# Kernel tuning notes

Hardware: AMD Instinct MI355X
Metric: run time of the kernel (lower is better)

The kernel has to match this reference:

```python
import jax, jax.numpy as jnp
import numpy as np

N = 50000
E = 1600000
F_IN = 256
HEADS = 4
HID = 32
C = 16
NEG_SLOPE = 0.2


def _add_self_loops(edge_index, n):
    loop = jnp.arange(n, dtype=edge_index.dtype)
    return jnp.concatenate([edge_index, jnp.stack([loop, loop])], axis=1)


def gat_conv(x, edge_index, W, att_src, att_dst, bias, heads, n):
    # PyG GATConv (concat=True, add_self_loops=True, inference: no dropout)
    ei = _add_self_loops(edge_index, n)
    src, dst = ei[0], ei[1]
    d = W.shape[1] // heads
    xw = (x @ W).reshape(n, heads, d)                      # [N,H,D]
    a_src = jnp.sum(xw * att_src, axis=-1)                 # [N,H]
    a_dst = jnp.sum(xw * att_dst, axis=-1)                 # [N,H]
    e = jax.nn.leaky_relu(a_src[src] + a_dst[dst], NEG_SLOPE)  # [E',H]
    # segment softmax over destination neighborhoods
    m = jax.ops.segment_max(e, dst, num_segments=n)        # [N,H]
    ex = jnp.exp(e - m[dst])
    denom = jax.ops.segment_sum(ex, dst, num_segments=n)   # [N,H]
    alpha = ex / denom[dst]                                # [E',H]
    msg = xw[src] * alpha[:, :, None]                      # [E',H,D]
    out = jax.ops.segment_sum(msg, dst, num_segments=n)    # [N,H,D]
    return out.reshape(n, heads * d) + bias


def setup_inputs() -> dict:
    key = jax.random.key(0)
    ks = jax.random.split(key, 10)
    g = lambda k, shape, fan: jax.random.normal(k, shape, jnp.float32) * (1.0 / np.sqrt(fan))
    x = jax.random.normal(ks[0], (N, F_IN), jnp.float32)
    edge_index = jax.random.randint(ks[1], (2, E), 0, N, dtype=jnp.int64)
    return {
        "x": x,
        "edge_index": edge_index,
        "W1": g(ks[2], (F_IN, HEADS * HID), F_IN),
        "att_src1": g(ks[3], (HEADS, HID), HID),
        "att_dst1": g(ks[4], (HEADS, HID), HID),
        "b1": jnp.zeros((HEADS * HID,), jnp.float32),
        "W2": g(ks[5], (HEADS * HID, C), HEADS * HID),
        "att_src2": g(ks[6], (1, C), C),
        "att_dst2": g(ks[7], (1, C), C),
        "b2": jnp.zeros((C,), jnp.float32),
    }


def reference(x, edge_index, W1, att_src1, att_dst1, b1, W2, att_src2, att_dst2, b2):
    h = gat_conv(x, edge_index, W1, att_src1, att_dst1, b1, HEADS, N)
    h = jax.nn.relu(h)
    # dropout: identity at inference (training=False)
    out = gat_conv(h, edge_index, W2, att_src2, att_dst2, b2, 1, N)
    return jax.nn.log_softmax(out, axis=1)
```

## Files before the change

kernel.cpp:

```cpp
#include <hip/hip_runtime.h>
#include <hip/hip_bf16.h>

typedef __hip_bfloat16 bf16;
typedef long long i64;
typedef unsigned long long u64;
typedef __attribute__((ext_vector_type(8))) short short8;
typedef __attribute__((ext_vector_type(4))) float floatx4;

#define NN    50000
#define EE    1600000
#define E2    1650000
#define FIN   256
#define HD    128
#define NH    4
#define NC    16
#define SLOPE 0.2f
#define K     128
#define DPB   391
#define CAPB  16384
#define CAP   15360
#define CH2   2048

#define FR_W  36
#define FW_W  68

#define OF_FLAGS 0
#define OF_BCUR  16
#define OF_BBASE 144
#define OF_RP    280
#define OF_BIN   50282
#define OF_CSR   4244586
#define OF_XQ    5894588
#define OF_SC    7494588
#define OF_AS1   9094588
#define OF_AD1   9294588
#define OF_HW2   9494588
#define OF_AS2   10294588
#define OF_AD2   10344588

__device__ __forceinline__ float b2f(bf16 v) { return __bfloat162float(v); }
__device__ __forceinline__ float us2f(unsigned short u) {
    return __uint_as_float(((unsigned)u) << 16);
}
__device__ __forceinline__ unsigned short f2us(float f) {
    unsigned u = __float_as_uint(f);
    return (unsigned short)((u + 0x7fffu + ((u >> 16) & 1u)) >> 16);
}
__device__ __forceinline__ float lrelu(float v) { return v > 0.f ? v : SLOPE * v; }
__device__ __forceinline__ float sb2f(unsigned u, int sh) {
    return (float)((int)(u << (24 - sh)) >> 24);
}

template <bool F32>
__device__ __forceinline__ float ldin(const void* p, int i) {
    if (F32) return ((const float*)p)[i];
    return b2f(((const bf16*)p)[i]);
}
template <bool F32>
__device__ __forceinline__ float4 ldin4(const void* p, int i) {
    if (F32) return *(const float4*)((const float*)p + i);
    ushort4 u = *(const ushort4*)((const unsigned short*)p + i);
    float4 r;
    r.x = us2f(u.x); r.y = us2f(u.y); r.z = us2f(u.z); r.w = us2f(u.w);
    return r;
}

__device__ __forceinline__ void edge_sd(const void* ei, int f64, int e, int& s, int& d) {
    if (e >= EE) { s = e - EE; d = s; return; }
    if (f64) {
        s = (int)((const i64*)ei)[e];
        d = (int)((const i64*)ei)[EE + e];
    } else {
        s = ((const int*)ei)[e];
        d = ((const int*)ei)[EE + e];
    }
    s = min(max(s, 0), NN - 1);
    d = min(max(d, 0), NN - 1);
}

__global__ void detect(const void* x, const void* ei, int* flags, int* bcur) {
    __shared__ int cnt[2];
    int t = threadIdx.x;
    if (t < K) bcur[t] = t * CAPB;
    if (t == 0) { cnt[0] = 0; cnt[1] = 0; }
    __syncthreads();
    const unsigned short* xb = (const unsigned short*)x;
    int c0 = 0;
    for (int i = t; i < 4096; i += 256) {
        float v = __uint_as_float(((unsigned)xb[2 * i]) << 16);
        if (!(fabsf(v) < 1e6f)) c0++;
    }
    const i64* e64 = (const i64*)ei;
    int c1 = 0;
    for (int i = t; i < 1024; i += 256) {
        i64 v = e64[i];
        if (v >= 0 && v < NN) c1++;
    }
    atomicAdd(&cnt[0], c0);
    atomicAdd(&cnt[1], c1);
    __syncthreads();
    if (t == 0) {
        flags[0] = (cnt[0] > 400) ? 1 : 0;
        flags[1] = (cnt[1] >= 1000) ? 1 : 0;
    }
}

__global__ __launch_bounds__(256) void binScatter(const void* __restrict__ ei,
                                                  const int* __restrict__ flags,
                                                  int* __restrict__ bcur,
                                                  u64* __restrict__ bin) {
    __shared__ int h[K], res[K];
    int t = threadIdx.x;
    int base = blockIdx.x * CH2 + t * 8;
    if (t < K) h[t] = 0;
    __syncthreads();
    int f64 = flags[1];
    int sv[8], dv[8], rk[8];
    int n_ = 0;
    if (!f64 && base + 8 <= EE) {
        const int* es = (const int*)ei;
        int4 a = *(const int4*)&es[base];
        int4 b = *(const int4*)&es[base + 4];
        int4 c = *(const int4*)&es[EE + base];
        int4 g = *(const int4*)&es[EE + base + 4];
        sv[0] = a.x; sv[1] = a.y; sv[2] = a.z; sv[3] = a.w;
        sv[4] = b.x; sv[5] = b.y; sv[6] = b.z; sv[7] = b.w;
        dv[0] = c.x; dv[1] = c.y; dv[2] = c.z; dv[3] = c.w;
        dv[4] = g.x; dv[5] = g.y; dv[6] = g.z; dv[7] = g.w;
#pragma unroll
        for (int i = 0; i < 8; i++) {
            sv[i] = min(max(sv[i], 0), NN - 1);
            dv[i] = min(max(dv[i], 0), NN - 1);
        }
        n_ = 8;
    } else {
        for (int i = 0; i < 8; i++) {
            int e = base + i;
            if (e < E2) {
                int s, d; edge_sd(ei, f64, e, s, d);
                sv[n_] = s; dv[n_] = d; n_++;
            }
        }
    }
#pragma unroll 8
    for (int i = 0; i < n_; i++) rk[i] = atomicAdd(&h[dv[i] / DPB], 1);
    __syncthreads();
    if (t < K) res[t] = h[t] ? atomicAdd(&bcur[t], h[t]) : 0;
    __syncthreads();
#pragma unroll 8
    for (int i = 0; i < n_; i++) {
        int b = dv[i] / DPB;
        int pos = res[b] + rk[i];
        pos = min(pos, (b + 1) * CAPB - 1);
        bin[pos] = (((u64)(unsigned)dv[i]) << 32) | (unsigned)sv[i];
    }
}

__global__ void bucketScan(const int* __restrict__ bcur, int* __restrict__ bbase) {
    __shared__ int sh[K];
    int t = threadIdx.x;
    int v = min(bcur[t] - t * CAPB, CAPB);
    sh[t] = v;
    __syncthreads();
    for (int off = 1; off < K; off <<= 1) {
        int u = (t >= off) ? sh[t - off] : 0;
        __syncthreads();
        sh[t] += u;
        __syncthreads();
    }
    bbase[t] = sh[t] - v;
    if (t == K - 1) bbase[K] = sh[K - 1];
}

__global__ __launch_bounds__(256) void csrB(const u64* __restrict__ bin,
                                            const int* __restrict__ bbase,
                                            int* __restrict__ rp, int* __restrict__ csr) {
    __shared__ int cnt[512];
    __shared__ int cur[DPB];
    __shared__ int buf[CAP];
    int b = blockIdx.x, t = threadIdx.x;
    int d0 = b * DPB;
    int nd = min(DPB, NN - d0);
    int src0 = b * CAPB;
    int base = bbase[b], size = bbase[b + 1] - base;
    cnt[t] = 0; cnt[t + 256] = 0;
    __syncthreads();
    for (int i = t; i < size; i += 256) {
        int d = (int)(bin[src0 + i] >> 32);
        atomicAdd(&cnt[d - d0], 1);
    }
    __syncthreads();
    int a0 = cnt[2 * t], a1 = cnt[2 * t + 1];
    int ps = a0 + a1;
    buf[t] = ps;
    __syncthreads();
    for (int off = 1; off < 256; off <<= 1) {
        int u = (t >= off) ? buf[t - off] : 0;
        __syncthreads();
        buf[t] += u;
        __syncthreads();
    }
    int ex = buf[t] - ps;
    __syncthreads();
    cnt[2 * t] = ex;
    cnt[2 * t + 1] = ex + a0;
    __syncthreads();
    for (int i = t; i < nd; i += 256) {
        rp[d0 + i] = base + cnt[i];
        cur[i] = cnt[i];
    }
    if (b == K - 1 && t == 0) rp[NN] = bbase[K];
    __syncthreads();
    if (size <= CAP) {
        for (int i = t; i < size; i += 256) {
            u64 p = bin[src0 + i];
            int pos = atomicAdd(&cur[(int)(p >> 32) - d0], 1);
            buf[pos] = (int)(unsigned)p;
        }
        __syncthreads();
        for (int i = t; i < size; i += 256) csr[base + i] = buf[i];
    } else {
        for (int i = t; i < size; i += 256) {
            u64 p = bin[src0 + i];
            int pos = base + atomicAdd(&cur[(int)(p >> 32) - d0], 1);
            csr[pos] = (int)(unsigned)p;
        }
    }
}

template <bool F32>
__global__ __launch_bounds__(256) void gemm1(
    const void* __restrict__ x, const void* __restrict__ W1,
    const void* __restrict__ as1, const void* __restrict__ ad1,
    const int* __restrict__ flags, signed char* __restrict__ xq, float* __restrict__ sc2,
    float* __restrict__ asrc, float* __restrict__ adst) {
    if ((flags[0] != 0) != F32) return;
    __shared__ unsigned short af[8 * 64 * FR_W];
    __shared__ unsigned short wb[8 * 64 * FR_W];
    __shared__ float scl[64];
    int t = threadIdx.x;
    int mb = blockIdx.x >> 1, nb = blockIdx.x & 1;
    int m0 = mb * 64, n0 = nb * 64;
#pragma unroll
    for (int i = 0; i < 16; i++) {
        int slot = i * 256 + t;
        int mi = slot >> 6, k4 = (slot & 63) * 4;
        float4 v = make_float4(0.f, 0.f, 0.f, 0.f);
        if (m0 + mi < NN) v = ldin4<F32>(x, (m0 + mi) * FIN + k4);
        ushort4 o;
        o.x = f2us(v.x); o.y = f2us(v.y); o.z = f2us(v.z); o.w = f2us(v.w);
        *(ushort4*)&af[((k4 >> 5) * 64 + mi) * FR_W + (k4 & 31)] = o;
    }
#pragma unroll
    for (int i = 0; i < 16; i++) {
        int k = i * 16 + (t >> 4);
        int ni = (t & 15) * 4;
        float4 v = ldin4<F32>(W1, k * HD + n0 + ni);
        int ks = k >> 5, kk = k & 31;
        wb[(ks * 64 + ni + 0) * FR_W + kk] = f2us(v.x);
        wb[(ks * 64 + ni + 1) * FR_W + kk] = f2us(v.y);
        wb[(ks * 64 + ni + 2) * FR_W + kk] = f2us(v.z);
        wb[(ks * 64 + ni + 3) * FR_W + kk] = f2us(v.w);
    }
    __syncthreads();
    int w = t >> 6, lane = t & 63;
    int col = lane & 15, q = lane >> 4;
    floatx4 dacc[4];
#pragma unroll
    for (int mt = 0; mt < 4; mt++) { dacc[mt].x = 0.f; dacc[mt].y = 0.f; dacc[mt].z = 0.f; dacc[mt].w = 0.f; }
#pragma unroll
    for (int ks = 0; ks < 8; ks++) {
        short8 bf = *(const short8*)&wb[(ks * 64 + w * 16 + col) * FR_W + q * 8];
#pragma unroll
        for (int mt = 0; mt < 4; mt++) {
            short8 afr = *(const short8*)&af[(ks * 64 + mt * 16 + col) * FR_W + q * 8];
            dacc[mt] = __builtin_amdgcn_mfma_f32_16x16x32_bf16(afr, bf, dacc[mt], 0, 0, 0);
        }
    }
    __syncthreads();
    float* fw = (float*)af;
#pragma unroll
    for (int mt = 0; mt < 4; mt++) {
#pragma unroll
        for (int r = 0; r < 4; r++) {
            int nloc = mt * 16 + q * 4 + r;
            fw[nloc * FW_W + w * 16 + col] = dacc[mt][r];
        }
    }
    __syncthreads();
    {
        int node = t >> 2, part = t & 3;
        float amax = 0.f;
#pragma unroll
        for (int c = 0; c < 16; c++) amax = fmaxf(amax, fabsf(fw[node * FW_W + part * 16 + c]));
        amax = fmaxf(amax, __shfl_xor(amax, 1));
        amax = fmaxf(amax, __shfl_xor(amax, 2));
        if (part == 0) {
            scl[node] = (amax > 0.f) ? 127.f / amax : 0.f;
            if (m0 + node < NN) sc2[(m0 + node) * 2 + nb] = amax * (1.f / 127.f);
        }
    }
    __syncthreads();
    {
        int node = t >> 2, part = t & 3;
        if (m0 + node < NN) {
            float inv = scl[node];
            unsigned dw[4];
#pragma unroll
            for (int g = 0; g < 4; g++) {
                unsigned pk = 0;
#pragma unroll
                for (int j = 0; j < 4; j++) {
                    float v = fw[node * FW_W + part * 16 + g * 4 + j];
                    int qi = (int)rintf(v * inv);
                    qi = min(127, max(-127, qi));
                    pk |= ((unsigned)(qi & 255)) << (8 * j);
                }
                dw[g] = pk;
            }
            *(uint4*)&xq[(m0 + node) * HD + n0 + part * 16] = make_uint4(dw[0], dw[1], dw[2], dw[3]);
        }
    }
    {
        int node = t >> 2, hh = (t >> 1) & 1, half = t & 1;
        if (m0 + node < NN) {
            float s = 0.f, dd = 0.f;
            int cb = hh * 32 + half * 16;
#pragma unroll
            for (int c = 0; c < 16; c++) {
                float xv = fw[node * FW_W + cb + c];
                s  += xv * ldin<F32>(as1, n0 + cb + c);
                dd += xv * ldin<F32>(ad1, n0 + cb + c);
            }
            s  += __shfl_xor(s, 1);
            dd += __shfl_xor(dd, 1);
            if (half == 0) {
                int head = nb * 2 + hh;
                asrc[(m0 + node) * NH + head] = s;
                adst[(m0 + node) * NH + head] = dd;
            }
        }
    }
}

template <bool F32>
__global__ __launch_bounds__(128) void node1(
    const int* __restrict__ rp, const int* __restrict__ cs,
    const float* __restrict__ asrc, const float* __restrict__ adst,
    const signed char* __restrict__ xq, const float* __restrict__ sc2,
    const void* __restrict__ b1, const void* __restrict__ W2,
    const void* __restrict__ as2, const void* __restrict__ ad2,
    const int* __restrict__ flags, float* __restrict__ hw2,
    float* __restrict__ asrc2, float* __restrict__ adst2) {
    if ((flags[0] != 0) != F32) return;
    int d = blockIdx.x, t = threadIdx.x;
    int beg = rp[d], end = rp[d + 1];
    __shared__ float sw[32][4];
    __shared__ int   ss[32];
    __shared__ float red[2][HD];
    __shared__ float wv[2][4];
    __shared__ float hs[HD];
    __shared__ float l2[32];
    int hw_ = t & 3;
    float adw = adst[d * NH + hw_];
    int cg = t & 15, eo = t >> 4, head = cg >> 2;
    float acc[8];
#pragma unroll
    for (int j = 0; j < 8; j++) acc[j] = 0.f;
    float wacc = 0.f;
    const unsigned* xqu = (const unsigned*)xq;
    for (int chb = beg; chb < end; chb += 32) {
        __syncthreads();
        int ec = chb + (t >> 2);
        float w = 0.f, wsc = 0.f;
        int s = 0;
        if (ec < end) {
            s = cs[ec];
            w = __expf(fminf(lrelu(asrc[s * NH + hw_] + adw), 80.f));
            wsc = w * sc2[s * 2 + (hw_ >> 1)];
        }
        sw[t >> 2][hw_] = wsc;
        if (hw_ == 0) ss[t >> 2] = s;
        wacc += w;
        __syncthreads();
        int m = min(32, end - chb);
        for (int e = eo; e < m; e += 8) {
            float we = sw[e][head];
            int s2 = ss[e];
            uint2 u = *(const uint2*)&xqu[s2 * 32 + cg * 2];
            acc[0] += we * sb2f(u.x, 0);
            acc[1] += we * sb2f(u.x, 8);
            acc[2] += we * sb2f(u.x, 16);
            acc[3] += we * sb2f(u.x, 24);
            acc[4] += we * sb2f(u.y, 0);
            acc[5] += we * sb2f(u.y, 8);
            acc[6] += we * sb2f(u.y, 16);
            acc[7] += we * sb2f(u.y, 24);
        }
    }
    wacc += __shfl_xor(wacc, 4);
    wacc += __shfl_xor(wacc, 8);
    wacc += __shfl_xor(wacc, 16);
    wacc += __shfl_xor(wacc, 32);
    int wid = t >> 6, lane = t & 63;
    if (lane < 4) wv[wid][lane] = wacc;
#pragma unroll
    for (int j = 0; j < 8; j++) {
        acc[j] += __shfl_xor(acc[j], 16);
        acc[j] += __shfl_xor(acc[j], 32);
    }
    if (lane < 16) {
#pragma unroll
        for (int j = 0; j < 8; j++) red[wid][lane * 8 + j] = acc[j];
    }
    __syncthreads();
    float tot = red[0][t] + red[1][t];
    float wt  = wv[0][t >> 5] + wv[1][t >> 5];
    hs[t] = fmaxf(tot / wt + ldin<F32>(b1, t), 0.f);
    __syncthreads();
    int j = t & 15, g = t >> 4;
    float p = 0.f;
#pragma unroll
    for (int k = 0; k < 16; k++) p += hs[g * 16 + k] * ldin<F32>(W2, (g * 16 + k) * NC + j);
    p += __shfl_xor(p, 16, 64);
    p += __shfl_xor(p, 32, 64);
    if ((t & 63) < 16) l2[(t >> 6) * 16 + j] = p;
    __syncthreads();
    if (t < 16) {
        float hw = l2[t] + l2[16 + t];
        hw2[d * NC + t] = hw;
        float a2s = hw * ldin<F32>(as2, t);
        float a2d = hw * ldin<F32>(ad2, t);
#pragma unroll
        for (int off = 8; off; off >>= 1) {
            a2s += __shfl_xor(a2s, off, 16);
            a2d += __shfl_xor(a2d, off, 16);
        }
        if (t == 0) { asrc2[d] = a2s; adst2[d] = a2d; }
    }
}

template <bool F32>
__global__ __launch_bounds__(64) void node2(
    const int* __restrict__ rp, const int* __restrict__ cs,
    const float* __restrict__ asrc2, const float* __restrict__ adst2,
    const float* __restrict__ hw2, const void* __restrict__ b2,
    const int* __restrict__ flags, void* __restrict__ out) {
    if ((flags[0] != 0) != F32) return;
    int d = blockIdx.x, t = threadIdx.x;
    int beg = rp[d], end = rp[d + 1];
    float ad = adst2[d];
    __shared__ float sw2[64];
    __shared__ int   ss2[64];
    int q = t & 3, eo = t >> 2;
    float4 acc = make_float4(0.f, 0.f, 0.f, 0.f);
    float wsum = 0.f;
    for (int chb = beg; chb < end; chb += 64) {
        __syncthreads();
        int ec = chb + t;
        float w = 0.f;
        int s = 0;
        if (ec < end) {
            s = cs[ec];
            w = __expf(fminf(lrelu(asrc2[s] + ad), 80.f));
        }
        sw2[t] = w;
        ss2[t] = s;
        __syncthreads();
        int m = min(64, end - chb);
        for (int e = eo; e < m; e += 16) {
            float we = sw2[e];
            float4 v = *(const float4*)&hw2[ss2[e] * NC + q * 4];
            acc.x += we * v.x; acc.y += we * v.y;
            acc.z += we * v.z; acc.w += we * v.w;
            wsum += we;
        }
    }
#pragma unroll
    for (int off = 4; off < 64; off <<= 1) {
        acc.x += __shfl_xor(acc.x, off);
        acc.y += __shfl_xor(acc.y, off);
        acc.z += __shfl_xor(acc.z, off);
        acc.w += __shfl_xor(acc.w, off);
        wsum  += __shfl_xor(wsum, off);
    }
    float rw = 1.f / wsum;
    float v0 = acc.x * rw + ldin<F32>(b2, q * 4 + 0);
    float v1 = acc.y * rw + ldin<F32>(b2, q * 4 + 1);
    float v2 = acc.z * rw + ldin<F32>(b2, q * 4 + 2);
    float v3 = acc.w * rw + ldin<F32>(b2, q * 4 + 3);
    float mx = fmaxf(fmaxf(v0, v1), fmaxf(v2, v3));
    mx = fmaxf(mx, __shfl_xor(mx, 1));
    mx = fmaxf(mx, __shfl_xor(mx, 2));
    float es = __expf(v0 - mx) + __expf(v1 - mx) + __expf(v2 - mx) + __expf(v3 - mx);
    es += __shfl_xor(es, 1);
    es += __shfl_xor(es, 2);
    float lse = mx + __logf(es);
    if (t < 4) {
        if (F32) {
            *(float4*)&((float*)out)[d * NC + q * 4] =
                make_float4(v0 - lse, v1 - lse, v2 - lse, v3 - lse);
        } else {
            bf16* o = (bf16*)out + d * NC + q * 4;
            o[0] = __float2bfloat16(v0 - lse); o[1] = __float2bfloat16(v1 - lse);
            o[2] = __float2bfloat16(v2 - lse); o[3] = __float2bfloat16(v3 - lse);
        }
    }
}

extern "C" void kernel_launch(void* const* d_in, const int* in_sizes, int n_in,
                              void* d_out, int out_size, void* d_ws, size_t ws_size,
                              hipStream_t stream) {
    const void* x   = d_in[0];
    const void* ei  = d_in[1];
    const void* W1  = d_in[2];
    const void* as1 = d_in[3];
    const void* ad1 = d_in[4];
    const void* b1  = d_in[5];
    const void* W2  = d_in[6];
    const void* as2 = d_in[7];
    const void* ad2 = d_in[8];
    const void* b2v = d_in[9];

    float* ws = (float*)d_ws;
    int* flags = (int*)(ws + OF_FLAGS);
    int* bcur  = (int*)(ws + OF_BCUR);
    int* bbase = (int*)(ws + OF_BBASE);
    int* rp    = (int*)(ws + OF_RP);
    u64* bin   = (u64*)(ws + OF_BIN);
    int* csr   = (int*)(ws + OF_CSR);
    signed char* xq = (signed char*)(ws + OF_XQ);
    float* sc2   = ws + OF_SC;
    float* asrc1 = ws + OF_AS1;
    float* adst1 = ws + OF_AD1;
    float* hw2   = ws + OF_HW2;
    float* asrc2 = ws + OF_AS2;
    float* adst2 = ws + OF_AD2;

    detect<<<1, 256, 0, stream>>>(x, ei, flags, bcur);
    binScatter<<<(E2 + CH2 - 1) / CH2, 256, 0, stream>>>(ei, flags, bcur, bin);
    bucketScan<<<1, K, 0, stream>>>(bcur, bbase);
    csrB<<<K, 256, 0, stream>>>(bin, bbase, rp, csr);

    const int GB = ((NN + 63) / 64) * 2;
    gemm1<true><<<GB, 256, 0, stream>>>(x, W1, as1, ad1, flags, xq, sc2, asrc1, adst1);
    node1<true><<<NN, 128, 0, stream>>>(rp, csr, asrc1, adst1, xq, sc2, b1, W2, as2, ad2,
                                        flags, hw2, asrc2, adst2);
    node2<true><<<NN, 64, 0, stream>>>(rp, csr, asrc2, adst2, hw2, b2v, flags, d_out);
}
```

Measured before the change: 306.2 us.

## Split layer-1 aggregation into per-half-head passes with wave-per-node and separate W2 kernel

Splits the int8 projected features into two 64-column halves so each of two aggregation passes gathers a smaller per-node working set that better fits in cache. Each wavefront handles one destination node, using ds_bpermute for broadcast instead of shared memory and block barriers. The W2 projection and layer-2 attention scores move into a separate kernel that handles 16 nodes per block with W2 cached in LDS. This costs an extra bf16 round trip for the hidden activations, reads the CSR twice, and adds kernel launches.

```diff
diff --git a/kernel.cpp b/kernel.cpp
--- a/kernel.cpp
+++ b/kernel.cpp
@@ -27,16 +27,19 @@
 #define OF_FLAGS 0
 #define OF_BCUR  16
 #define OF_BBASE 144
-#define OF_RP    280
-#define OF_BIN   50282
-#define OF_CSR   4244586
-#define OF_XQ    5894588
-#define OF_SC    7494588
-#define OF_AS1   9094588
-#define OF_AD1   9294588
-#define OF_HW2   9494588
-#define OF_AS2   10294588
-#define OF_AD2   10344588
+#define OF_RP    304
+#define OF_BIN   50308
+#define OF_HA    50308
+#define OF_HB    1650308
+#define OF_CSR   4244612
+#define OF_XQA   5894612
+#define OF_XQB   6694612
+#define OF_SC    7494612
+#define OF_AS1   7594612
+#define OF_AD1   7794612
+#define OF_HW2   7994612
+#define OF_AS2   8794612
+#define OF_AD2   8844612
 
 __device__ __forceinline__ float b2f(bf16 v) { return __bfloat162float(v); }
 __device__ __forceinline__ float us2f(unsigned short u) {
@@ -49,6 +52,12 @@
 __device__ __forceinline__ float lrelu(float v) { return v > 0.f ? v : SLOPE * v; }
 __device__ __forceinline__ float sb2f(unsigned u, int sh) {
     return (float)((int)(u << (24 - sh)) >> 24);
+}
+__device__ __forceinline__ float bpermf(int srcLane, float v) {
+    return __int_as_float(__builtin_amdgcn_ds_bpermute(srcLane * 4, __float_as_int(v)));
+}
+__device__ __forceinline__ int bpermi(int srcLane, int v) {
+    return __builtin_amdgcn_ds_bpermute(srcLane * 4, v);
 }
 
 template <bool F32>
@@ -232,9 +241,10 @@
 __global__ __launch_bounds__(256) void gemm1(
     const void* __restrict__ x, const void* __restrict__ W1,
     const void* __restrict__ as1, const void* __restrict__ ad1,
-    const int* __restrict__ flags, signed char* __restrict__ xq, float* __restrict__ sc2,
+    const int* __restrict__ flags, signed char* __restrict__ xqA,
+    signed char* __restrict__ xqB, float* __restrict__ sc2,
     float* __restrict__ asrc, float* __restrict__ adst) {
-    if ((flags[0] != 0) != F32) return;
+    if (flags[0] != (F32 ? 1 : 0)) return;
     __shared__ unsigned short af[8 * 64 * FR_W];
     __shared__ unsigned short wb[8 * 64 * FR_W];
     __shared__ float scl[64];
@@ -318,7 +328,8 @@
                 }
                 dw[g] = pk;
             }
-            *(uint4*)&xq[(m0 + node) * HD + n0 + part * 16] = make_uint4(dw[0], dw[1], dw[2], dw[3]);
+            signed char* xqH = nb ? xqB : xqA;
+            *(uint4*)&xqH[(m0 + node) * 64 + part * 16] = make_uint4(dw[0], dw[1], dw[2], dw[3]);
         }
     }
     {
@@ -343,101 +354,116 @@
     }
 }
 
-template <bool F32>
-__global__ __launch_bounds__(128) void node1(
+template <bool F32, int HALF>
+__global__ __launch_bounds__(256) void nodeAgg(
     const int* __restrict__ rp, const int* __restrict__ cs,
     const float* __restrict__ asrc, const float* __restrict__ adst,
-    const signed char* __restrict__ xq, const float* __restrict__ sc2,
-    const void* __restrict__ b1, const void* __restrict__ W2,
-    const void* __restrict__ as2, const void* __restrict__ ad2,
-    const int* __restrict__ flags, float* __restrict__ hw2,
-    float* __restrict__ asrc2, float* __restrict__ adst2) {
-    if ((flags[0] != 0) != F32) return;
-    int d = blockIdx.x, t = threadIdx.x;
+    const signed char* __restrict__ xqH, const float* __restrict__ sc2,
+    const void* __restrict__ b1, const int* __restrict__ flags,
+    unsigned short* __restrict__ hH) {
+    if (flags[0] != (F32 ? 1 : 0)) return;
+    int t = threadIdx.x, wv = t >> 6, lane = t & 63;
+    int d = blockIdx.x * 4 + wv;
     int beg = rp[d], end = rp[d + 1];
-    __shared__ float sw[32][4];
-    __shared__ int   ss[32];
-    __shared__ float red[2][HD];
-    __shared__ float wv[2][4];
-    __shared__ float hs[HD];
-    __shared__ float l2[32];
-    int hw_ = t & 3;
-    float adw = adst[d * NH + hw_];
-    int cg = t & 15, eo = t >> 4, head = cg >> 2;
+    int eloc = lane >> 1, h = lane & 1;
+    int cg = lane & 7, eo = lane >> 3, hl = cg >> 2;
+    float adw = adst[d * NH + HALF * 2 + h];
+    const unsigned* xqu = (const unsigned*)xqH;
     float acc[8];
 #pragma unroll
     for (int j = 0; j < 8; j++) acc[j] = 0.f;
     float wacc = 0.f;
-    const unsigned* xqu = (const unsigned*)xq;
-    for (int chb = beg; chb < end; chb += 32) {
-        __syncthreads();
-        int ec = chb + (t >> 2);
-        float w = 0.f, wsc = 0.f;
+    for (int ch = beg; ch < end; ch += 32) {
+        int idx = ch + eloc;
+        float wsc = 0.f;
         int s = 0;
-        if (ec < end) {
-            s = cs[ec];
-            w = __expf(fminf(lrelu(asrc[s * NH + hw_] + adw), 80.f));
-            wsc = w * sc2[s * 2 + (hw_ >> 1)];
-        }
-        sw[t >> 2][hw_] = wsc;
-        if (hw_ == 0) ss[t >> 2] = s;
-        wacc += w;
-        __syncthreads();
-        int m = min(32, end - chb);
-        for (int e = eo; e < m; e += 8) {
-            float we = sw[e][head];
-            int s2 = ss[e];
-            uint2 u = *(const uint2*)&xqu[s2 * 32 + cg * 2];
-            acc[0] += we * sb2f(u.x, 0);
-            acc[1] += we * sb2f(u.x, 8);
-            acc[2] += we * sb2f(u.x, 16);
-            acc[3] += we * sb2f(u.x, 24);
-            acc[4] += we * sb2f(u.y, 0);
-            acc[5] += we * sb2f(u.y, 8);
-            acc[6] += we * sb2f(u.y, 16);
-            acc[7] += we * sb2f(u.y, 24);
-        }
-    }
+        if (idx < end) {
+            s = cs[idx];
+            float wval = __expf(fminf(lrelu(asrc[s * NH + HALF * 2 + h] + adw), 80.f));
+            wacc += wval;
+            wsc = wval * sc2[s * 2 + HALF];
+        }
+        int m = min(32, end - ch);
+        int rounds = (m + 7) >> 3;
+        for (int r = 0; r < rounds; r++) {
+            int e = eo + r * 8;
+            float we = bpermf(e * 2 + hl, wsc);
+            int s2 = bpermi(e * 2, s);
+            if (e < m) {
+                uint2 u = *(const uint2*)&xqu[s2 * 16 + cg * 2];
+                acc[0] += we * sb2f(u.x, 0);
+                acc[1] += we * sb2f(u.x, 8);
+                acc[2] += we * sb2f(u.x, 16);
+                acc[3] += we * sb2f(u.x, 24);
+                acc[4] += we * sb2f(u.y, 0);
+                acc[5] += we * sb2f(u.y, 8);
+                acc[6] += we * sb2f(u.y, 16);
+                acc[7] += we * sb2f(u.y, 24);
+            }
+        }
+    }
+#pragma unroll
+    for (int j = 0; j < 8; j++) {
+        acc[j] += __shfl_xor(acc[j], 8);
+        acc[j] += __shfl_xor(acc[j], 16);
+        acc[j] += __shfl_xor(acc[j], 32);
+    }
+    wacc += __shfl_xor(wacc, 2);
     wacc += __shfl_xor(wacc, 4);
     wacc += __shfl_xor(wacc, 8);
     wacc += __shfl_xor(wacc, 16);
     wacc += __shfl_xor(wacc, 32);
-    int wid = t >> 6, lane = t & 63;
-    if (lane < 4) wv[wid][lane] = wacc;
-#pragma unroll
-    for (int j = 0; j < 8; j++) {
-        acc[j] += __shfl_xor(acc[j], 16);
-        acc[j] += __shfl_xor(acc[j], 32);
-    }
-    if (lane < 16) {
-#pragma unroll
-        for (int j = 0; j < 8; j++) red[wid][lane * 8 + j] = acc[j];
-    }
-    __syncthreads();
-    float tot = red[0][t] + red[1][t];
-    float wt  = wv[0][t >> 5] + wv[1][t >> 5];
-    hs[t] = fmaxf(tot / wt + ldin<F32>(b1, t), 0.f);
-    __syncthreads();
-    int j = t & 15, g = t >> 4;
-    float p = 0.f;
-#pragma unroll
-    for (int k = 0; k < 16; k++) p += hs[g * 16 + k] * ldin<F32>(W2, (g * 16 + k) * NC + j);
-    p += __shfl_xor(p, 16, 64);
-    p += __shfl_xor(p, 32, 64);
-    if ((t & 63) < 16) l2[(t >> 6) * 16 + j] = p;
-    __syncthreads();
-    if (t < 16) {
-        float hw = l2[t] + l2[16 + t];
-        hw2[d * NC + t] = hw;
-        float a2s = hw * ldin<F32>(as2, t);
-        float a2d = hw * ldin<F32>(ad2, t);
-#pragma unroll
-        for (int off = 8; off; off >>= 1) {
-            a2s += __shfl_xor(a2s, off, 16);
-            a2d += __shfl_xor(a2d, off, 16);
-        }
-        if (t == 0) { asrc2[d] = a2s; adst2[d] = a2d; }
-    }
+    float ws0 = __shfl(wacc, 0), ws1 = __shfl(wacc, 1);
+    if (eo == 0) {
+        float rw = 1.f / (hl ? ws1 : ws0);
+        unsigned pk[4];
+#pragma unroll
+        for (int g = 0; g < 4; g++) {
+            float v0 = fmaxf(acc[2 * g]     * rw + ldin<F32>(b1, HALF * 64 + cg * 8 + 2 * g), 0.f);
+            float v1 = fmaxf(acc[2 * g + 1] * rw + ldin<F32>(b1, HALF * 64 + cg * 8 + 2 * g + 1), 0.f);
+            pk[g] = ((unsigned)f2us(v1) << 16) | f2us(v0);
+        }
+        *(uint4*)&hH[(size_t)d * 64 + cg * 8] = make_uint4(pk[0], pk[1], pk[2], pk[3]);
+    }
+}
+
+template <bool F32>
+__global__ __launch_bounds__(256) void nodeW(
+    const unsigned short* __restrict__ hA, const unsigned short* __restrict__ hB,
+    const void* __restrict__ W2, const void* __restrict__ as2, const void* __restrict__ ad2,
+    const int* __restrict__ flags, float* __restrict__ hw2,
+    float* __restrict__ asrc2, float* __restrict__ adst2) {
+    if (flags[0] != (F32 ? 1 : 0)) return;
+    __shared__ float hs[16][132];
+    __shared__ float w2s[HD * NC];
+    int t = threadIdx.x;
+    int dst0 = blockIdx.x * 16;
+    for (int i = t; i < HD * NC / 4; i += 256)
+        *(float4*)&w2s[i * 4] = ldin4<F32>(W2, i * 4);
+    {
+        int dn = t >> 4, oct = t & 15;
+        uint4 u = (oct < 8) ? ((const uint4*)hA)[(size_t)(dst0 + dn) * 8 + oct]
+                            : ((const uint4*)hB)[(size_t)(dst0 + dn) * 8 + (oct - 8)];
+        float* hp = &hs[dn][oct * 8];
+        hp[0] = us2f((unsigned short)(u.x & 0xffff)); hp[1] = us2f((unsigned short)(u.x >> 16));
+        hp[2] = us2f((unsigned short)(u.y & 0xffff)); hp[3] = us2f((unsigned short)(u.y >> 16));
+        hp[4] = us2f((unsigned short)(u.z & 0xffff)); hp[5] = us2f((unsigned short)(u.z >> 16));
+        hp[6] = us2f((unsigned short)(u.w & 0xffff)); hp[7] = us2f((unsigned short)(u.w >> 16));
+    }
+    __syncthreads();
+    int ln = t >> 4, j = t & 15;
+    float acc = 0.f;
+#pragma unroll 8
+    for (int k = 0; k < HD; k++) acc += hs[ln][k] * w2s[k * NC + j];
+    hw2[(dst0 + ln) * NC + j] = acc;
+    float a2s = acc * ldin<F32>(as2, j);
+    float a2d = acc * ldin<F32>(ad2, j);
+#pragma unroll
+    for (int off = 8; off; off >>= 1) {
+        a2s += __shfl_xor(a2s, off, 16);
+        a2d += __shfl_xor(a2d, off, 16);
+    }
+    if (j == 0) { asrc2[dst0 + ln] = a2s; adst2[dst0 + ln] = a2d; }
 }
 
 template <bool F32>
@@ -446,7 +472,7 @@
     const float* __restrict__ asrc2, const float* __restrict__ adst2,
     const float* __restrict__ hw2, const void* __restrict__ b2,
     const int* __restrict__ flags, void* __restrict__ out) {
-    if ((flags[0] != 0) != F32) return;
+    if (flags[0] != (F32 ? 1 : 0)) return;
     int d = blockIdx.x, t = threadIdx.x;
     int beg = rp[d], end = rp[d + 1];
     float ad = adst2[d];
@@ -529,7 +555,10 @@
     int* rp    = (int*)(ws + OF_RP);
     u64* bin   = (u64*)(ws + OF_BIN);
     int* csr   = (int*)(ws + OF_CSR);
-    signed char* xq = (signed char*)(ws + OF_XQ);
+    signed char* xqA = (signed char*)(ws + OF_XQA);
+    signed char* xqB = (signed char*)(ws + OF_XQB);
+    unsigned short* hA = (unsigned short*)(ws + OF_HA);
+    unsigned short* hB = (unsigned short*)(ws + OF_HB);
     float* sc2   = ws + OF_SC;
     float* asrc1 = ws + OF_AS1;
     float* adst1 = ws + OF_AD1;
@@ -543,8 +572,9 @@
     csrB<<<K, 256, 0, stream>>>(bin, bbase, rp, csr);
 
     const int GB = ((NN + 63) / 64) * 2;
-    gemm1<true><<<GB, 256, 0, stream>>>(x, W1, as1, ad1, flags, xq, sc2, asrc1, adst1);
-    node1<true><<<NN, 128, 0, stream>>>(rp, csr, asrc1, adst1, xq, sc2, b1, W2, as2, ad2,
-                                        flags, hw2, asrc2, adst2);
+    gemm1<true><<<GB, 256, 0, stream>>>(x, W1, as1, ad1, flags, xqA, xqB, sc2, asrc1, adst1);
+    nodeAgg<true, 0><<<NN / 4, 256, 0, stream>>>(rp, csr, asrc1, adst1, xqA, sc2, b1, flags, hA);
+    nodeAgg<true, 1><<<NN / 4, 256, 0, stream>>>(rp, csr, asrc1, adst1, xqB, sc2, b1, flags, hB);
+    nodeW<true><<<NN / 16, 256, 0, stream>>>(hA, hB, W2, as2, ad2, flags, hw2, asrc2, adst2);
     node2<true><<<NN, 64, 0, stream>>>(rp, csr, asrc2, adst2, hw2, b2v, flags, d_out);
 }
```

Result: slower. 324.8 us (+6.1%).

## Pretranspose W1 once and compute full 128-column tile per gemm1 block

Applied to the files above, without the earlier changes.

Adds a small kernel that converts W1 to bf16 in an MFMA-friendly transposed layout in workspace. gemm1 then reads B fragments straight from global memory instead of staging W1 in shared memory. Each block now covers all 128 output columns for its 64 rows, so the x tile is loaded and converted once per row instead of twice. The epilogue, quantization and attention dot products are reworked to match. In exchange, each wave holds more accumulator registers and does more global B-fragment reads.

```diff
diff --git a/kernel.cpp b/kernel.cpp
--- a/kernel.cpp
+++ b/kernel.cpp
@@ -21,22 +21,22 @@
 #define CAP   15360
 #define CH2   2048
 
-#define FR_W  36
-#define FW_W  68
+#define KS_S  2312
 
 #define OF_FLAGS 0
 #define OF_BCUR  16
 #define OF_BBASE 144
 #define OF_RP    280
-#define OF_BIN   50282
-#define OF_CSR   4244586
-#define OF_XQ    5894588
-#define OF_SC    7494588
-#define OF_AS1   9094588
-#define OF_AD1   9294588
-#define OF_HW2   9494588
-#define OF_AS2   10294588
-#define OF_AD2   10344588
+#define OF_W1T   50284
+#define OF_BIN   66668
+#define OF_CSR   4260972
+#define OF_XQ    5910972
+#define OF_SC    7510972
+#define OF_AS1   7610972
+#define OF_AD1   7810972
+#define OF_HW2   8010972
+#define OF_AS2   8810972
+#define OF_AD2   8860972
 
 __device__ __forceinline__ float b2f(bf16 v) { return __bfloat162float(v); }
 __device__ __forceinline__ float us2f(unsigned short u) {
@@ -49,6 +49,9 @@
 __device__ __forceinline__ float lrelu(float v) { return v > 0.f ? v : SLOPE * v; }
 __device__ __forceinline__ float sb2f(unsigned u, int sh) {
     return (float)((int)(u << (24 - sh)) >> 24);
+}
+__device__ __forceinline__ int fwi(int node, int ch) {
+    return node * 132 + (ch >> 5) * 33 + (ch & 31);
 }
 
 template <bool F32>
@@ -103,6 +106,20 @@
         flags[0] = (cnt[0] > 400) ? 1 : 0;
         flags[1] = (cnt[1] >= 1000) ? 1 : 0;
     }
+}
+
+template <bool F32>
+__global__ void trW(const void* __restrict__ W1, const int* __restrict__ flags,
+                    unsigned short* __restrict__ w1t) {
+    if (flags[0] != (F32 ? 1 : 0)) return;
+    int t = blockIdx.x * 256 + threadIdx.x;
+    int k = t >> 5, n4 = (t & 31) * 4;
+    float4 v = ldin4<F32>(W1, k * HD + n4);
+    int ks = k >> 5, kk = k & 31;
+    w1t[((ks * HD + n4 + 0) * 32) + kk] = f2us(v.x);
+    w1t[((ks * HD + n4 + 1) * 32) + kk] = f2us(v.y);
+    w1t[((ks * HD + n4 + 2) * 32) + kk] = f2us(v.z);
+    w1t[((ks * HD + n4 + 3) * 32) + kk] = f2us(v.w);
 }
 
 __global__ __launch_bounds__(256) void binScatter(const void* __restrict__ ei,
@@ -230,17 +247,15 @@
 
 template <bool F32>
 __global__ __launch_bounds__(256) void gemm1(
-    const void* __restrict__ x, const void* __restrict__ W1,
+    const void* __restrict__ x, const unsigned short* __restrict__ w1t,
     const void* __restrict__ as1, const void* __restrict__ ad1,
     const int* __restrict__ flags, signed char* __restrict__ xq, float* __restrict__ sc2,
     float* __restrict__ asrc, float* __restrict__ adst) {
-    if ((flags[0] != 0) != F32) return;
-    __shared__ unsigned short af[8 * 64 * FR_W];
-    __shared__ unsigned short wb[8 * 64 * FR_W];
-    __shared__ float scl[64];
+    if (flags[0] != (F32 ? 1 : 0)) return;
+    __shared__ unsigned short af[8 * KS_S];
+    __shared__ float scl[128];
     int t = threadIdx.x;
-    int mb = blockIdx.x >> 1, nb = blockIdx.x & 1;
-    int m0 = mb * 64, n0 = nb * 64;
+    int m0 = blockIdx.x * 64;
 #pragma unroll
     for (int i = 0; i < 16; i++) {
         int slot = i * 256 + t;
@@ -249,97 +264,77 @@
         if (m0 + mi < NN) v = ldin4<F32>(x, (m0 + mi) * FIN + k4);
         ushort4 o;
         o.x = f2us(v.x); o.y = f2us(v.y); o.z = f2us(v.z); o.w = f2us(v.w);
-        *(ushort4*)&af[((k4 >> 5) * 64 + mi) * FR_W + (k4 & 31)] = o;
-    }
-#pragma unroll
-    for (int i = 0; i < 16; i++) {
-        int k = i * 16 + (t >> 4);
-        int ni = (t & 15) * 4;
-        float4 v = ldin4<F32>(W1, k * HD + n0 + ni);
-        int ks = k >> 5, kk = k & 31;
-        wb[(ks * 64 + ni + 0) * FR_W + kk] = f2us(v.x);
-        wb[(ks * 64 + ni + 1) * FR_W + kk] = f2us(v.y);
-        wb[(ks * 64 + ni + 2) * FR_W + kk] = f2us(v.z);
-        wb[(ks * 64 + ni + 3) * FR_W + kk] = f2us(v.w);
+        *(ushort4*)&af[(k4 >> 5) * KS_S + mi * 36 + (k4 & 31)] = o;
     }
     __syncthreads();
     int w = t >> 6, lane = t & 63;
     int col = lane & 15, q = lane >> 4;
-    floatx4 dacc[4];
-#pragma unroll
-    for (int mt = 0; mt < 4; mt++) { dacc[mt].x = 0.f; dacc[mt].y = 0.f; dacc[mt].z = 0.f; dacc[mt].w = 0.f; }
+    floatx4 acc[4][2];
+#pragma unroll
+    for (int mt = 0; mt < 4; mt++)
+#pragma unroll
+        for (int u = 0; u < 2; u++) { acc[mt][u].x = 0.f; acc[mt][u].y = 0.f; acc[mt][u].z = 0.f; acc[mt][u].w = 0.f; }
 #pragma unroll
     for (int ks = 0; ks < 8; ks++) {
-        short8 bf = *(const short8*)&wb[(ks * 64 + w * 16 + col) * FR_W + q * 8];
+        short8 bf0 = *(const short8*)&w1t[(ks * HD + w * 32 + col) * 32 + q * 8];
+        short8 bf1 = *(const short8*)&w1t[(ks * HD + w * 32 + 16 + col) * 32 + q * 8];
 #pragma unroll
         for (int mt = 0; mt < 4; mt++) {
-            short8 afr = *(const short8*)&af[(ks * 64 + mt * 16 + col) * FR_W + q * 8];
-            dacc[mt] = __builtin_amdgcn_mfma_f32_16x16x32_bf16(afr, bf, dacc[mt], 0, 0, 0);
+            short8 afr = *(const short8*)&af[ks * KS_S + (mt * 16 + col) * 36 + q * 8];
+            acc[mt][0] = __builtin_amdgcn_mfma_f32_16x16x32_bf16(afr, bf0, acc[mt][0], 0, 0, 0);
+            acc[mt][1] = __builtin_amdgcn_mfma_f32_16x16x32_bf16(afr, bf1, acc[mt][1], 0, 0, 0);
         }
     }
     __syncthreads();
     float* fw = (float*)af;
 #pragma unroll
-    for (int mt = 0; mt < 4; mt++) {
-#pragma unroll
-        for (int r = 0; r < 4; r++) {
-            int nloc = mt * 16 + q * 4 + r;
-            fw[nloc * FW_W + w * 16 + col] = dacc[mt][r];
-        }
-    }
-    __syncthreads();
+    for (int mt = 0; mt < 4; mt++)
+#pragma unroll
+        for (int u = 0; u < 2; u++)
+#pragma unroll
+            for (int r = 0; r < 4; r++) {
+                int node = mt * 16 + q * 4 + r;
+                fw[fwi(node, w * 32 + u * 16 + col)] = acc[mt][u][r];
+            }
+    __syncthreads();
+    int node = t >> 2, part = t & 3;
     {
-        int node = t >> 2, part = t & 3;
         float amax = 0.f;
 #pragma unroll
-        for (int c = 0; c < 16; c++) amax = fmaxf(amax, fabsf(fw[node * FW_W + part * 16 + c]));
+        for (int c = 0; c < 32; c++) amax = fmaxf(amax, fabsf(fw[fwi(node, part * 32 + c)]));
         amax = fmaxf(amax, __shfl_xor(amax, 1));
-        amax = fmaxf(amax, __shfl_xor(amax, 2));
-        if (part == 0) {
-            scl[node] = (amax > 0.f) ? 127.f / amax : 0.f;
-            if (m0 + node < NN) sc2[(m0 + node) * 2 + nb] = amax * (1.f / 127.f);
-        }
-    }
-    __syncthreads();
-    {
-        int node = t >> 2, part = t & 3;
-        if (m0 + node < NN) {
-            float inv = scl[node];
-            unsigned dw[4];
-#pragma unroll
-            for (int g = 0; g < 4; g++) {
-                unsigned pk = 0;
-#pragma unroll
-                for (int j = 0; j < 4; j++) {
-                    float v = fw[node * FW_W + part * 16 + g * 4 + j];
-                    int qi = (int)rintf(v * inv);
-                    qi = min(127, max(-127, qi));
-                    pk |= ((unsigned)(qi & 255)) << (8 * j);
-                }
-                dw[g] = pk;
+        if ((part & 1) == 0) {
+            scl[node * 2 + (part >> 1)] = (amax > 0.f) ? 127.f / amax : 0.f;
+            if (m0 + node < NN) sc2[(m0 + node) * 2 + (part >> 1)] = amax * (1.f / 127.f);
+        }
+    }
+    __syncthreads();
+    if (m0 + node < NN) {
+        float inv = scl[node * 2 + (part >> 1)];
+        unsigned dw[8];
+#pragma unroll
+        for (int g = 0; g < 8; g++) {
+            unsigned pk = 0;
+#pragma unroll
+            for (int j = 0; j < 4; j++) {
+                float v = fw[fwi(node, part * 32 + g * 4 + j)];
+                int qi = (int)rintf(v * inv);
+                qi = min(127, max(-127, qi));
+                pk |= ((unsigned)(qi & 255)) << (8 * j);
             }
-            *(uint4*)&xq[(m0 + node) * HD + n0 + part * 16] = make_uint4(dw[0], dw[1], dw[2], dw[3]);
-        }
-    }
-    {
-        int node = t >> 2, hh = (t >> 1) & 1, half = t & 1;
-        if (m0 + node < NN) {
-            float s = 0.f, dd = 0.f;
-            int cb = hh * 32 + half * 16;
-#pragma unroll
-            for (int c = 0; c < 16; c++) {
-                float xv = fw[node * FW_W + cb + c];
-                s  += xv * ldin<F32>(as1, n0 + cb + c);
-                dd += xv * ldin<F32>(ad1, n0 + cb + c);
-            }
-            s  += __shfl_xor(s, 1);
-            dd += __shfl_xor(dd, 1);
-            if (half == 0) {
-                int head = nb * 2 + hh;
-                asrc[(m0 + node) * NH + head] = s;
-                adst[(m0 + node) * NH + head] = dd;
-            }
-        }
+            dw[g] = pk;
+        }
+        *(uint4*)&xq[(m0 + node) * HD + part * 32]      = make_uint4(dw[0], dw[1], dw[2], dw[3]);
+        *(uint4*)&xq[(m0 + node) * HD + part * 32 + 16] = make_uint4(dw[4], dw[5], dw[6], dw[7]);
+        float s = 0.f, dd = 0.f;
+#pragma unroll
+        for (int c = 0; c < 32; c++) {
+            float xv = fw[fwi(node, part * 32 + c)];
+            s  += xv * ldin<F32>(as1, part * 32 + c);
+            dd += xv * ldin<F32>(ad1, part * 32 + c);
+        }
+        asrc[(m0 + node) * NH + part] = s;
+        adst[(m0 + node) * NH + part] = dd;
     }
 }
 
@@ -352,7 +347,7 @@
     const void* __restrict__ as2, const void* __restrict__ ad2,
     const int* __restrict__ flags, float* __restrict__ hw2,
     float* __restrict__ asrc2, float* __restrict__ adst2) {
-    if ((flags[0] != 0) != F32) return;
+    if (flags[0] != (F32 ? 1 : 0)) return;
     int d = blockIdx.x, t = threadIdx.x;
     int beg = rp[d], end = rp[d + 1];
     __shared__ float sw[32][4];
@@ -446,7 +441,7 @@
     const float* __restrict__ asrc2, const float* __restrict__ adst2,
     const float* __restrict__ hw2, const void* __restrict__ b2,
     const int* __restrict__ flags, void* __restrict__ out) {
-    if ((flags[0] != 0) != F32) return;
+    if (flags[0] != (F32 ? 1 : 0)) return;
     int d = blockIdx.x, t = threadIdx.x;
     int beg = rp[d], end = rp[d + 1];
     float ad = adst2[d];
@@ -527,6 +522,7 @@
     int* bcur  = (int*)(ws + OF_BCUR);
     int* bbase = (int*)(ws + OF_BBASE);
     int* rp    = (int*)(ws + OF_RP);
+    unsigned short* w1t = (unsigned short*)(ws + OF_W1T);
     u64* bin   = (u64*)(ws + OF_BIN);
     int* csr   = (int*)(ws + OF_CSR);
     signed char* xq = (signed char*)(ws + OF_XQ);
@@ -538,12 +534,13 @@
     float* adst2 = ws + OF_AD2;
 
     detect<<<1, 256, 0, stream>>>(x, ei, flags, bcur);
+    trW<true><<<32, 256, 0, stream>>>(W1, flags, w1t);
     binScatter<<<(E2 + CH2 - 1) / CH2, 256, 0, stream>>>(ei, flags, bcur, bin);
     bucketScan<<<1, K, 0, stream>>>(bcur, bbase);
     csrB<<<K, 256, 0, stream>>>(bin, bbase, rp, csr);
 
-    const int GB = ((NN + 63) / 64) * 2;
-    gemm1<true><<<GB, 256, 0, stream>>>(x, W1, as1, ad1, flags, xq, sc2, asrc1, adst1);
+    const int GB = (NN + 63) / 64;
+    gemm1<true><<<GB, 256, 0, stream>>>(x, w1t, as1, ad1, flags, xq, sc2, asrc1, adst1);
     node1<true><<<NN, 128, 0, stream>>>(rp, csr, asrc1, adst1, xq, sc2, b1, W2, as2, ad2,
                                         flags, hw2, asrc2, adst2);
     node2<true><<<NN, 64, 0, stream>>>(rp, csr, asrc2, adst2, hw2, b2v, flags, d_out);
```

New measurement: 295.3 us. -3.5%, faster.
